# Performance work log

Hardware: AMD Instinct MI355X
Metric: run time of the kernel (lower is better)

## Reference

```python
import jax, jax.numpy as jnp
import numpy as np

IN, H, HC, HQ, OUT = 7, 64, 32, 16, 3  # input, shared hidden, cell hidden, head hidden, per-task out
B, S = 256, 2048


def setup_inputs() -> dict:
    key = jax.random.key(0)
    ks = iter(jax.random.split(key, 40))
    def p(shape, scale=0.1):
        return jax.random.normal(next(ks), shape, dtype=jnp.float32) * scale
    d = {}
    d['x'] = jax.random.normal(next(ks), (B, S, IN), dtype=jnp.float32)
    # shared LSTM (torch gate order i,f,g,o)
    d['W_ih_s'] = p((4 * H, IN)); d['W_hh_s'] = p((4 * H, H))
    d['b_ih_s'] = p((4 * H,));    d['b_hh_s'] = p((4 * H,))
    # attitude cell: input = [shared_h(64), x(7)]
    d['W_ih_a'] = p((4 * HC, H + IN)); d['W_hh_a'] = p((4 * HC, HC))
    d['b_ih_a'] = p((4 * HC,));        d['b_hh_a'] = p((4 * HC,))
    # velocity cell: input = [shared_h(64), delta_att(3), x(7)]
    d['W_ih_v'] = p((4 * HC, H + OUT + IN)); d['W_hh_v'] = p((4 * HC, HC))
    d['b_ih_v'] = p((4 * HC,));              d['b_hh_v'] = p((4 * HC,))
    # position cell: input = [shared_h(64), delta_vel(3)]
    d['W_ih_p'] = p((4 * HC, H + OUT)); d['W_hh_p'] = p((4 * HC, HC))
    d['b_ih_p'] = p((4 * HC,));         d['b_hh_p'] = p((4 * HC,))
    # per-task readout MLPs (dropout is identity in eval mode)
    d['Wa1'] = p((HQ, HC)); d['ba1'] = p((HQ,)); d['Wa2'] = p((OUT, HQ)); d['ba2'] = p((OUT,))
    d['Wv1'] = p((HQ, HC)); d['bv1'] = p((HQ,)); d['Wv2'] = p((OUT, HQ)); d['bv2'] = p((OUT,))
    d['Wp1'] = p((HQ, HC)); d['bp1'] = p((HQ,)); d['Wp2'] = p((OUT, HQ)); d['bp2'] = p((OUT,))
    return d


def lstm_cell(x, h, c, Wih, Whh, bih, bhh):
    z = x @ Wih.T + h @ Whh.T + bih + bhh
    i, f, g, o = jnp.split(z, 4, axis=-1)
    c = jax.nn.sigmoid(f) * c + jax.nn.sigmoid(i) * jnp.tanh(g)
    h = jax.nn.sigmoid(o) * jnp.tanh(c)
    return h, c


def mlp(h, W1, b1, W2, b2):
    return jax.nn.relu(h @ W1.T + b1) @ W2.T + b2


def reference(x, W_ih_s, W_hh_s, b_ih_s, b_hh_s,
              W_ih_a, W_hh_a, b_ih_a, b_hh_a,
              W_ih_v, W_hh_v, b_ih_v, b_hh_v,
              W_ih_p, W_hh_p, b_ih_p, b_hh_p,
              Wa1, ba1, Wa2, ba2, Wv1, bv1, Wv2, bv2, Wp1, bp1, Wp2, bp2):
    b = x.shape[0]
    z = lambda n: jnp.zeros((b, n), x.dtype)
    carry0 = (z(H), z(H), z(HC), z(HC), z(HC), z(HC), z(HC), z(HC))

    def step(carry, xt):
        hs, cs, ha, ca, hv, cv, hp, cp = carry
        hs, cs = lstm_cell(xt, hs, cs, W_ih_s, W_hh_s, b_ih_s, b_hh_s)
        ha, ca = lstm_cell(jnp.concatenate([hs, xt], -1), ha, ca,
                           W_ih_a, W_hh_a, b_ih_a, b_hh_a)
        d_att = mlp(ha, Wa1, ba1, Wa2, ba2)
        hv, cv = lstm_cell(jnp.concatenate([hs, jax.lax.stop_gradient(d_att), xt], -1),
                           hv, cv, W_ih_v, W_hh_v, b_ih_v, b_hh_v)
        d_vel = mlp(hv, Wv1, bv1, Wv2, bv2)
        hp, cp = lstm_cell(jnp.concatenate([hs, jax.lax.stop_gradient(d_vel)], -1),
                           hp, cp, W_ih_p, W_hh_p, b_ih_p, b_hh_p)
        d_pos = mlp(hp, Wp1, bp1, Wp2, bp2)
        out = jnp.concatenate([d_att, d_vel, d_pos], -1)  # [B, 9]
        return (hs, cs, ha, ca, hv, cv, hp, cp), out

    _, ys = jax.lax.scan(step, carry0, jnp.swapaxes(x, 0, 1))  # [S, B, 9]
    return jnp.swapaxes(ys, 0, 1)  # [B, S, 9]
```

## Files before the change

kernel.cpp:

```cpp
#include <hip/hip_runtime.h>

typedef unsigned int u32;

#define NIN 7
#define NB 256
#define NS 2048

__device__ __forceinline__ float fastrcp(float x){ return __builtin_amdgcn_rcpf(x); }
__device__ __forceinline__ float sigf(float x){ return fastrcp(1.f + __expf(-x)); }
__device__ __forceinline__ float tanhf_(float x){ return 1.f - 2.f*fastrcp(1.f + __expf(2.f*x)); }

__device__ __forceinline__ u32 pkh(float a, float b){
  unsigned short ua = __builtin_bit_cast(unsigned short, (_Float16)a);
  unsigned short ub = __builtin_bit_cast(unsigned short, (_Float16)b);
  return (u32)ua | ((u32)ub << 16);
}

template<int J>
__device__ __forceinline__ float rlf(float v){
  return __uint_as_float((unsigned)__builtin_amdgcn_readlane((int)__float_as_uint(v), J));
}
__device__ __forceinline__ float rlfv(float v, int j){
  return __uint_as_float((unsigned)__builtin_amdgcn_readlane((int)__float_as_uint(v), j));
}

__device__ __forceinline__ float mxl(float acc, u32 wp, float a){
  asm("v_fma_mix_f32 %0, %1, %2, %3 op_sel_hi:[1,0,0]"
      : "=v"(acc) : "v"(wp), "s"(a), "0"(acc));
  return acc;
}
__device__ __forceinline__ float mxh(float acc, u32 wp, float a){
  asm("v_fma_mix_f32 %0, %1, %2, %3 op_sel:[1,0,0] op_sel_hi:[1,0,0]"
      : "=v"(acc) : "v"(wp), "s"(a), "0"(acc));
  return acc;
}
__device__ __forceinline__ float mxlv(float acc, u32 wp, float a){
  asm("v_fma_mix_f32 %0, %1, %2, %3 op_sel_hi:[1,0,0]"
      : "=v"(acc) : "v"(wp), "v"(a), "0"(acc));
  return acc;
}
__device__ __forceinline__ float mxhv(float acc, u32 wp, float a){
  asm("v_fma_mix_f32 %0, %1, %2, %3 op_sel:[1,0,0] op_sel_hi:[1,0,0]"
      : "=v"(acc) : "v"(wp), "v"(a), "0"(acc));
  return acc;
}

__device__ __forceinline__ float gate4(float zi, float zf, float zg, float zo, float& c){
  c = sigf(zf)*c + sigf(zi)*tanhf_(zg);
  return sigf(zo)*tanhf_(c);
}

#define XD(a0, a1, KB, v0, v1) { \
  a0 = mxlv(a0, w[(KB)+0], (v0).x); a1 = mxhv(a1, w[(KB)+0], (v0).y); \
  a0 = mxlv(a0, w[(KB)+1], (v0).z); a1 = mxhv(a1, w[(KB)+1], (v0).w); \
  a0 = mxlv(a0, w[(KB)+2], (v1).x); a1 = mxhv(a1, w[(KB)+2], (v1).y); \
  a0 = mxlv(a0, w[(KB)+3], (v1).z); a1 = mxhv(a1, w[(KB)+3], (v1).w); }

#define LMX2(a0, a1, s0, s1, KA, KS, H4) { _Pragma("unroll") \
  for (int c_ = 0; c_ < 16; c_++){ \
    float4 h_ = (H4)[c_]; \
    a0 = mxlv(a0, w[(KA)+2*c_],   h_.x); a1 = mxhv(a1, w[(KA)+2*c_],   h_.y); \
    a0 = mxlv(a0, w[(KA)+2*c_+1], h_.z); a1 = mxhv(a1, w[(KA)+2*c_+1], h_.w); \
    s0 = mxlv(s0, w[(KS)+2*c_],   h_.x); s1 = mxhv(s1, w[(KS)+2*c_],   h_.y); \
    s0 = mxlv(s0, w[(KS)+2*c_+1], h_.z); s1 = mxhv(s1, w[(KS)+2*c_+1], h_.w); } }

#define LMX1(a0, a1, KA, H4) { _Pragma("unroll") \
  for (int c_ = 0; c_ < 16; c_++){ \
    float4 h_ = (H4)[c_]; \
    a0 = mxlv(a0, w[(KA)+2*c_],   h_.x); a1 = mxhv(a1, w[(KA)+2*c_],   h_.y); \
    a0 = mxlv(a0, w[(KA)+2*c_+1], h_.z); a1 = mxhv(a1, w[(KA)+2*c_+1], h_.w); } }

#define LMXH(z0, z1, KB, H4) { _Pragma("unroll") \
  for (int c_ = 0; c_ < 8; c_++){ \
    float4 h_ = (H4)[c_]; \
    z0 = mxlv(z0, w[(KB)+2*c_],   h_.x); z1 = mxhv(z1, w[(KB)+2*c_],   h_.y); \
    z0 = mxlv(z0, w[(KB)+2*c_+1], h_.z); z1 = mxhv(z1, w[(KB)+2*c_+1], h_.w); } }

#define MX2(a0, a1, s0, s1, KA, KS, SRC) { _Pragma("unroll") \
  for (int k_ = 0; k_ < 32; k_++){ \
    float e0_ = rlfv(SRC, 2*k_), e1_ = rlfv(SRC, 2*k_+1); \
    a0 = mxl(a0, w[(KA)+k_], e0_); a1 = mxh(a1, w[(KA)+k_], e1_); \
    s0 = mxl(s0, w[(KS)+k_], e0_); s1 = mxh(s1, w[(KS)+k_], e1_); } }

#define MX1(a0, a1, KA, SRC) { _Pragma("unroll") \
  for (int k_ = 0; k_ < 32; k_++){ \
    float e0_ = rlfv(SRC, 2*k_), e1_ = rlfv(SRC, 2*k_+1); \
    a0 = mxl(a0, w[(KA)+k_], e0_); a1 = mxh(a1, w[(KA)+k_], e1_); } }

#define MLPX(HS_, M1B, B1V, M2B, B2V, dres) { \
  float q0_ = (B1V), q1_ = 0.f, q2_ = 0.f, q3_ = 0.f; \
  _Pragma("unroll") \
  for (int j_ = 0; j_ < 16; j_++){ \
    float e0_ = rlfv(HS_, 2*j_), e1_ = rlfv(HS_, 2*j_+1); \
    if ((j_&1)==0){ q0_ = mxl(q0_, w[(M1B)+j_], e0_); q1_ = mxh(q1_, w[(M1B)+j_], e1_); } \
    else          { q2_ = mxl(q2_, w[(M1B)+j_], e0_); q3_ = mxh(q3_, w[(M1B)+j_], e1_); } } \
  float qq_ = fmaxf((q0_+q2_) + (q1_+q3_), 0.f); \
  float f0_ = (B2V), f1_ = 0.f, f2_ = 0.f, f3_ = 0.f; \
  _Pragma("unroll") \
  for (int j_ = 0; j_ < 8; j_++){ \
    float e0_ = rlfv(qq_, 2*j_), e1_ = rlfv(qq_, 2*j_+1); \
    if ((j_&1)==0){ f0_ = mxl(f0_, w[(M2B)+j_], e0_); f1_ = mxh(f1_, w[(M2B)+j_], e1_); } \
    else          { f2_ = mxl(f2_, w[(M2B)+j_], e0_); f3_ = mxh(f3_, w[(M2B)+j_], e1_); } } \
  dres = (f0_+f2_) + (f1_+f3_); }

__global__ __attribute__((amdgpu_flat_work_group_size(512,512), amdgpu_waves_per_eu(2,2)))
void mtinn_kernel(
    const float* __restrict__ x,
    const float* wihs, const float* whhs, const float* bihs, const float* bhhs,
    const float* wiha, const float* whha, const float* biha, const float* bhha,
    const float* wihv, const float* whhv, const float* bihv, const float* bhhv,
    const float* wihp, const float* whhp, const float* bihp, const float* bhhp,
    const float* wa1, const float* ba1, const float* wa2, const float* ba2,
    const float* wv1, const float* bv1, const float* wv2, const float* bv2,
    const float* wp1, const float* bp1, const float* wp2, const float* bp2,
    float* __restrict__ out)
{
  __shared__ __align__(16) float ZS[2][256];
  __shared__ __align__(16) float ZC[3][128];
  __shared__ __align__(16) float HS[64];
  __shared__ __align__(16) float HA[32], HV[32];
  __shared__ __align__(16) float HPb[2][32];
  __shared__ __align__(16) float XL[4][8];

  const int tid  = threadIdx.x;
  const int wave = tid >> 6, lane = tid & 63, l = lane & 31;
  const int b    = blockIdx.x;
  const float* xb = x + (size_t)b * NS * NIN;

  const bool isWin = (wave != 0 && wave != 4);
  const int  wc    = (wave==1||wave==7) ? 0 : (wave==2||wave==5) ? 1 : 2;
  const int  wrb   = (wave <= 3) ? 64 : 0;
  const bool isSh  = (wave==1 || wave==2 || wave==6 || wave==7);
  const int  qoff  = (wave==1) ? 0 : (wave==2) ? 64 : (wave==6) ? 128 : 192;
  const int  mi = lane & 15, mm = lane % 3;

  u32 w[88];
#pragma unroll
  for (int i = 0; i < 88; i++) w[i] = 0u;
  float b1a=0.f,b2a=0.f,b1v=0.f,b2v=0.f,b1p=0.f,b2p=0.f;

  if (isWin){
    const float* wih = (wc==0) ? wiha : (wc==1) ? wihv : wihp;
    const float* whh = (wc==0) ? whha : (wc==1) ? whhv : whhp;
    const float* bi  = (wc==0) ? biha : (wc==1) ? bihv : bihp;
    const float* bh  = (wc==0) ? bhha : (wc==1) ? bhhv : bhhp;
    const int L = (wc==0) ? 71 : (wc==1) ? 74 : 67;
    const int r = wrb + lane;
#pragma unroll
    for (int k=0;k<16;k++) w[k] = pkh(whh[r*32+2*k], whh[r*32+2*k+1]);
#pragma unroll
    for (int k=0;k<32;k++) w[16+k] = pkh(wih[r*L+2*k], wih[r*L+2*k+1]);
    const float bsum = bi[r] + bh[r];
    if (wc==0){
      w[48]=pkh(wih[r*L+64],wih[r*L+65]); w[49]=pkh(wih[r*L+66],wih[r*L+67]);
      w[50]=pkh(wih[r*L+68],wih[r*L+69]); w[51]=pkh(wih[r*L+70], bsum);
    } else if (wc==1){
      w[48]=pkh(wih[r*L+67],wih[r*L+68]); w[49]=pkh(wih[r*L+69],wih[r*L+70]);
      w[50]=pkh(wih[r*L+71],wih[r*L+72]); w[51]=pkh(wih[r*L+73], bsum);
    } else {
      w[51]=pkh(0.f, bsum);
    }
  }
  if (isSh){
    const int r = qoff + lane;
#pragma unroll
    for (int k=0;k<32;k++) w[52+k] = pkh(whhs[r*64+2*k], whhs[r*64+2*k+1]);
    w[84]=pkh(wihs[r*7+0],wihs[r*7+1]); w[85]=pkh(wihs[r*7+2],wihs[r*7+3]);
    w[86]=pkh(wihs[r*7+4],wihs[r*7+5]); w[87]=pkh(wihs[r*7+6], bihs[r]+bhhs[r]);
  }
  if (wave == 0){
#pragma unroll
    for (int k=0;k<16;k++){
      w[k]    = pkh(wa1[mi*32+2*k], wa1[mi*32+2*k+1]);
      w[16+k] = pkh(wv1[mi*32+2*k], wv1[mi*32+2*k+1]);
    }
#pragma unroll
    for (int k=0;k<8;k++){
      w[48+k] = pkh(wa2[mm*16+2*k], wa2[mm*16+2*k+1]);
      w[56+k] = pkh(wv2[mm*16+2*k], wv2[mm*16+2*k+1]);
    }
#pragma unroll
    for (int g=0; g<4; g++){
      int rr = g*32 + l;
      w[72+2*g]   = pkh(wihv[rr*74+64], wihv[rr*74+65]);
      w[72+2*g+1] = pkh(wihv[rr*74+66], 0.f);
      w[80+2*g]   = pkh(wihp[rr*67+64], wihp[rr*67+65]);
      w[80+2*g+1] = pkh(wihp[rr*67+66], 0.f);
    }
    b1a=ba1[mi]; b2a=ba2[mm]; b1v=bv1[mi]; b2v=bv2[mm];
  }
  if (wave == 4){
#pragma unroll
    for (int k=0;k<16;k++) w[k] = pkh(wp1[mi*32+2*k], wp1[mi*32+2*k+1]);
#pragma unroll
    for (int k=0;k<8;k++)  w[16+k] = pkh(wp2[mm*16+2*k], wp2[mm*16+2*k+1]);
    b1p=bp1[mi]; b2p=bp2[mm];
  }

  if (tid < 32) HA[tid]=0.f;
  else if (tid < 64)  HV[tid-32]=0.f;
  else if (tid < 96)  HPb[0][tid-64]=0.f;
  else if (tid < 128) HPb[1][tid-96]=0.f;
  if (tid < 8){
    XL[0][tid] = (tid<7) ? xb[tid]         : 1.f;
    XL[1][tid] = (tid<7) ? xb[NIN+tid]     : 1.f;
    XL[2][tid] = (tid<7) ? xb[2*NIN+tid]   : 1.f;
    XL[3][tid] = 1.f;
  }
  __syncthreads();

  if (isSh){
    const float4* X0 = (const float4*)XL[0];
    float4 xa = X0[0], xb4 = X0[1];
    float s0=0.f, s1=0.f; XD(s0,s1,84,xa,xb4);
    ZS[0][qoff + lane] = s0 + s1;
  }
  __syncthreads();

  float c_s = 0.f;
  float c_a = 0.f, c_v = 0.f, c_p = 0.f;
  float zpart = 0.f;

  if (isWin){
    float zi_=ZS[0][lane], zf_=ZS[0][64+lane], zg_=ZS[0][128+lane], zo_=ZS[0][192+lane];
    float hsv = gate4(zi_,zf_,zg_,zo_, c_s);
    const float4* X0 = (const float4*)XL[0];
    float4 xa = X0[0], xb4 = X0[1];
    float a0=0.f, a1=0.f; XD(a0,a1,48,xa,xb4);
    if (isSh){
      const float4* X1 = (const float4*)XL[1];
      float4 xc = X1[0], xd = X1[1];
      float s0=0.f, s1=0.f; XD(s0,s1,84,xc,xd);
      MX2(a0,a1,s0,s1,16,52,hsv);
      ZS[1][qoff + lane] = s0 + s1;
    } else {
      MX1(a0,a1,16,hsv);
    }
    zpart = a0 + a1;
  } else if (wave == 4){
    float zi_=ZS[0][lane], zf_=ZS[0][64+lane], zg_=ZS[0][128+lane], zo_=ZS[0][192+lane];
    gate4(zi_,zf_,zg_,zo_, c_s);
  }
  __syncthreads();

#pragma unroll 1
  for (int t = 0; t < NS; t++){
    float xpre = 0.f;
    if (wave == 0){
      if (lane < 7){
        const int tf = (t+3 < NS) ? t+3 : NS-1;
        xpre = xb[(size_t)tf*NIN + lane];
      }
    } else if (wave == 4){
      const float* Zsrc = ZS[(t+1)&1];
      float zi_=Zsrc[lane], zf_=Zsrc[64+lane], zg_=Zsrc[128+lane], zo_=Zsrc[192+lane];
      float hsv2 = gate4(zi_,zf_,zg_,zo_, c_s);
      HS[lane] = hsv2;
      if (t > 0){
        float hp_ = HPb[(t^1)&1][l];
        float dP; MLPX(hp_, 0, b1p, 16, b2p, dP);
        if (lane < 3) out[((size_t)b*NS + (t-1))*9 + 6 + lane] = dP;
      }
    } else {
      const float4* H4 = (const float4*)((wc==0) ? HA : (wc==1) ? HV : HPb[(t^1)&1]);
      float z0 = zpart, z1 = 0.f;
      LMXH(z0,z1,0,H4);
      ZC[wc][wrb + lane] = z0 + z1;
    }
    __syncthreads();

    if (wave == 0){
      __builtin_amdgcn_s_setprio(1);
      float zai=ZC[0][l], zaf=ZC[0][32+l], zag=ZC[0][64+l], zao=ZC[0][96+l];
      float zvi=ZC[1][l], zvf=ZC[1][32+l], zvg=ZC[1][64+l], zvo=ZC[1][96+l];
      float zpi=ZC[2][l], zpf=ZC[2][32+l], zpg=ZC[2][64+l], zpo=ZC[2][96+l];
      float* ob = out + ((size_t)b*NS + t)*9;
      float ha = gate4(zai,zaf,zag,zao, c_a);
      if (lane < 32) HA[lane] = ha;
      float dA; MLPX(ha, 0, b1a, 48, b2a, dA);
      if (lane < 3) ob[lane] = dA;
      float dx=rlf<0>(dA), dy=rlf<1>(dA), dz=rlf<2>(dA);
      zvi = mxl(zvi, w[72], dx); zvi = mxh(zvi, w[72], dy); zvi = mxl(zvi, w[73], dz);
      zvf = mxl(zvf, w[74], dx); zvf = mxh(zvf, w[74], dy); zvf = mxl(zvf, w[75], dz);
      zvg = mxl(zvg, w[76], dx); zvg = mxh(zvg, w[76], dy); zvg = mxl(zvg, w[77], dz);
      zvo = mxl(zvo, w[78], dx); zvo = mxh(zvo, w[78], dy); zvo = mxl(zvo, w[79], dz);
      float hv = gate4(zvi,zvf,zvg,zvo, c_v);
      if (lane < 32) HV[lane] = hv;
      float dV; MLPX(hv, 16, b1v, 56, b2v, dV);
      if (lane < 3) ob[3+lane] = dV;
      dx=rlf<0>(dV); dy=rlf<1>(dV); dz=rlf<2>(dV);
      zpi = mxl(zpi, w[80], dx); zpi = mxh(zpi, w[80], dy); zpi = mxl(zpi, w[81], dz);
      zpf = mxl(zpf, w[82], dx); zpf = mxh(zpf, w[82], dy); zpf = mxl(zpf, w[83], dz);
      zpg = mxl(zpg, w[84], dx); zpg = mxh(zpg, w[84], dy); zpg = mxl(zpg, w[85], dz);
      zpo = mxl(zpo, w[86], dx); zpo = mxh(zpo, w[86], dy); zpo = mxl(zpo, w[87], dz);
      float hp_ = gate4(zpi,zpf,zpg,zpo, c_p);
      if (lane < 32) HPb[t&1][lane] = hp_;
      __builtin_amdgcn_s_setprio(0);
      if (lane < 7) XL[(t+3)&3][lane] = xpre;
    } else if (isWin){
      const float4* H4 = (const float4*)HS;
      const float4* X1 = (const float4*)XL[(t+1)&3];
      float4 xa = X1[0], xb4 = X1[1];
      float a0=0.f, a1=0.f; XD(a0,a1,48,xa,xb4);
      if (isSh){
        const float4* X2 = (const float4*)XL[(t+2)&3];
        float4 xc = X2[0], xd = X2[1];
        float s0=0.f, s1=0.f; XD(s0,s1,84,xc,xd);
        LMX2(a0,a1,s0,s1,16,52,H4);
        ZS[t&1][qoff + lane] = s0 + s1;
      } else {
        LMX1(a0,a1,16,H4);
      }
      zpart = a0 + a1;
    }
    __syncthreads();
  }

  if (wave == 4){
    float hp_ = HPb[(NS-1)&1][l];
    float dP; MLPX(hp_, 0, b1p, 16, b2p, dP);
    if (lane < 3) out[((size_t)b*NS + (NS-1))*9 + 6 + lane] = dP;
  }
}

extern "C" void kernel_launch(void* const* d_in, const int* in_sizes, int n_in,
                              void* d_out, int out_size, void* d_ws, size_t ws_size,
                              hipStream_t stream) {
  (void)in_sizes; (void)n_in; (void)d_ws; (void)ws_size; (void)out_size;
  const float* X    = (const float*)d_in[0];
  const float* Wihs = (const float*)d_in[1];
  const float* Whhs = (const float*)d_in[2];
  const float* Bihs = (const float*)d_in[3];
  const float* Bhhs = (const float*)d_in[4];
  const float* Wiha = (const float*)d_in[5];
  const float* Whha = (const float*)d_in[6];
  const float* Biha = (const float*)d_in[7];
  const float* Bhha = (const float*)d_in[8];
  const float* Wihv = (const float*)d_in[9];
  const float* Whhv = (const float*)d_in[10];
  const float* Bihv = (const float*)d_in[11];
  const float* Bhhv = (const float*)d_in[12];
  const float* Wihp = (const float*)d_in[13];
  const float* Whhp = (const float*)d_in[14];
  const float* Bihp = (const float*)d_in[15];
  const float* Bhhp = (const float*)d_in[16];
  const float* Wa1  = (const float*)d_in[17];
  const float* Ba1  = (const float*)d_in[18];
  const float* Wa2  = (const float*)d_in[19];
  const float* Ba2  = (const float*)d_in[20];
  const float* Wv1  = (const float*)d_in[21];
  const float* Bv1  = (const float*)d_in[22];
  const float* Wv2  = (const float*)d_in[23];
  const float* Bv2  = (const float*)d_in[24];
  const float* Wp1  = (const float*)d_in[25];
  const float* Bp1  = (const float*)d_in[26];
  const float* Wp2  = (const float*)d_in[27];
  const float* Bp2  = (const float*)d_in[28];
  float* OUTP = (float*)d_out;

  mtinn_kernel<<<dim3(NB), dim3(512), 0, stream>>>(
      X, Wihs, Whhs, Bihs, Bhhs,
      Wiha, Whha, Biha, Bhha,
      Wihv, Whhv, Bihv, Bhhv,
      Wihp, Whhp, Bihp, Bhhp,
      Wa1, Ba1, Wa2, Ba2, Wv1, Bv1, Wv2, Bv2, Wp1, Bp1, Wp2, Bp2,
      OUTP);
}
```

Baseline: 2.935 ms.

## Rebalance shared-LSTM recurrent matvec across all cell waves with K-split partial sums

Instead of four cell waves each computing a full 64-row shared-LSTM gate block, the i/f/g rows are split across six cell waves by halves of the hidden dimension, with partial sums stored to separate LDS buffers and added by the gate wave. Wave 4 now also computes the output-gate rows of the shared LSTM. This evens out per-wave FMA work in the second phase to shorten the critical path and cuts the weight register array from 88 to 72 entries. The cost is extra LDS reads and adds in the gate step. The launch bounds attribute changes and the s_setprio priority boost for wave 0 is removed, which may hurt the serial head chain.

```diff
diff --git a/kernel.cpp b/kernel.cpp
--- a/kernel.cpp
+++ b/kernel.cpp
@@ -56,14 +56,6 @@
   a0 = mxlv(a0, w[(KB)+2], (v1).x); a1 = mxhv(a1, w[(KB)+2], (v1).y); \
   a0 = mxlv(a0, w[(KB)+3], (v1).z); a1 = mxhv(a1, w[(KB)+3], (v1).w); }
 
-#define LMX2(a0, a1, s0, s1, KA, KS, H4) { _Pragma("unroll") \
-  for (int c_ = 0; c_ < 16; c_++){ \
-    float4 h_ = (H4)[c_]; \
-    a0 = mxlv(a0, w[(KA)+2*c_],   h_.x); a1 = mxhv(a1, w[(KA)+2*c_],   h_.y); \
-    a0 = mxlv(a0, w[(KA)+2*c_+1], h_.z); a1 = mxhv(a1, w[(KA)+2*c_+1], h_.w); \
-    s0 = mxlv(s0, w[(KS)+2*c_],   h_.x); s1 = mxhv(s1, w[(KS)+2*c_],   h_.y); \
-    s0 = mxlv(s0, w[(KS)+2*c_+1], h_.z); s1 = mxhv(s1, w[(KS)+2*c_+1], h_.w); } }
-
 #define LMX1(a0, a1, KA, H4) { _Pragma("unroll") \
   for (int c_ = 0; c_ < 16; c_++){ \
     float4 h_ = (H4)[c_]; \
@@ -76,16 +68,20 @@
     z0 = mxlv(z0, w[(KB)+2*c_],   h_.x); z1 = mxhv(z1, w[(KB)+2*c_],   h_.y); \
     z0 = mxlv(z0, w[(KB)+2*c_+1], h_.z); z1 = mxhv(z1, w[(KB)+2*c_+1], h_.w); } }
 
-#define MX2(a0, a1, s0, s1, KA, KS, SRC) { _Pragma("unroll") \
-  for (int k_ = 0; k_ < 32; k_++){ \
-    float e0_ = rlfv(SRC, 2*k_), e1_ = rlfv(SRC, 2*k_+1); \
-    a0 = mxl(a0, w[(KA)+k_], e0_); a1 = mxh(a1, w[(KA)+k_], e1_); \
-    s0 = mxl(s0, w[(KS)+k_], e0_); s1 = mxh(s1, w[(KS)+k_], e1_); } }
-
 #define MX1(a0, a1, KA, SRC) { _Pragma("unroll") \
   for (int k_ = 0; k_ < 32; k_++){ \
     float e0_ = rlfv(SRC, 2*k_), e1_ = rlfv(SRC, 2*k_+1); \
     a0 = mxl(a0, w[(KA)+k_], e0_); a1 = mxh(a1, w[(KA)+k_], e1_); } }
+
+#define MXH16(z0, z1, KB, SRC) { _Pragma("unroll") \
+  for (int k_ = 0; k_ < 16; k_++){ \
+    float e0_ = rlfv(SRC, 2*k_), e1_ = rlfv(SRC, 2*k_+1); \
+    z0 = mxl(z0, w[(KB)+k_], e0_); z1 = mxh(z1, w[(KB)+k_], e1_); } }
+
+#define MXH16HI(z0, z1, KB, SRC) { _Pragma("unroll") \
+  for (int k_ = 0; k_ < 16; k_++){ \
+    float e0_ = rlfv(SRC, 32+2*k_), e1_ = rlfv(SRC, 33+2*k_); \
+    z0 = mxl(z0, w[(KB)+k_], e0_); z1 = mxh(z1, w[(KB)+k_], e1_); } }
 
 #define MLPX(HS_, M1B, B1V, M2B, B2V, dres) { \
   float q0_ = (B1V), q1_ = 0.f, q2_ = 0.f, q3_ = 0.f; \
@@ -103,8 +99,7 @@
     else          { f2_ = mxl(f2_, w[(M2B)+j_], e0_); f3_ = mxh(f3_, w[(M2B)+j_], e1_); } } \
   dres = (f0_+f2_) + (f1_+f3_); }
 
-__global__ __attribute__((amdgpu_flat_work_group_size(512,512), amdgpu_waves_per_eu(2,2)))
-void mtinn_kernel(
+__global__ __launch_bounds__(512, 1) void mtinn_kernel(
     const float* __restrict__ x,
     const float* wihs, const float* whhs, const float* bihs, const float* bhhs,
     const float* wiha, const float* whha, const float* biha, const float* bhha,
@@ -115,7 +110,9 @@
     const float* wp1, const float* bp1, const float* wp2, const float* bp2,
     float* __restrict__ out)
 {
-  __shared__ __align__(16) float ZS[2][256];
+  __shared__ __align__(16) float ZSL[2][192];
+  __shared__ __align__(16) float ZSH[2][192];
+  __shared__ __align__(16) float ZSO[2][64];
   __shared__ __align__(16) float ZC[3][128];
   __shared__ __align__(16) float HS[64];
   __shared__ __align__(16) float HA[32], HV[32];
@@ -130,13 +127,13 @@
   const bool isWin = (wave != 0 && wave != 4);
   const int  wc    = (wave==1||wave==7) ? 0 : (wave==2||wave==5) ? 1 : 2;
   const int  wrb   = (wave <= 3) ? 64 : 0;
-  const bool isSh  = (wave==1 || wave==2 || wave==6 || wave==7);
-  const int  qoff  = (wave==1) ? 0 : (wave==2) ? 64 : (wave==6) ? 128 : 192;
+  const bool shHi  = (wave >= 5);
+  const int  qoff  = (wave==1||wave==5) ? 0 : (wave==2||wave==6) ? 64 : 128;
   const int  mi = lane & 15, mm = lane % 3;
 
-  u32 w[88];
-#pragma unroll
-  for (int i = 0; i < 88; i++) w[i] = 0u;
+  u32 w[72];
+#pragma unroll
+  for (int i = 0; i < 72; i++) w[i] = 0u;
   float b1a=0.f,b2a=0.f,b1v=0.f,b2v=0.f,b1p=0.f,b2p=0.f;
 
   if (isWin){
@@ -160,13 +157,16 @@
     } else {
       w[51]=pkh(0.f, bsum);
     }
-  }
-  if (isSh){
-    const int r = qoff + lane;
-#pragma unroll
-    for (int k=0;k<32;k++) w[52+k] = pkh(whhs[r*64+2*k], whhs[r*64+2*k+1]);
-    w[84]=pkh(wihs[r*7+0],wihs[r*7+1]); w[85]=pkh(wihs[r*7+2],wihs[r*7+3]);
-    w[86]=pkh(wihs[r*7+4],wihs[r*7+5]); w[87]=pkh(wihs[r*7+6], bihs[r]+bhhs[r]);
+    const int rs = qoff + lane;
+    if (!shHi){
+#pragma unroll
+      for (int k=0;k<16;k++) w[52+k] = pkh(whhs[rs*64+2*k], whhs[rs*64+2*k+1]);
+    } else {
+#pragma unroll
+      for (int k=0;k<16;k++) w[52+k] = pkh(whhs[rs*64+32+2*k], whhs[rs*64+33+2*k]);
+      w[68]=pkh(wihs[rs*7+0],wihs[rs*7+1]); w[69]=pkh(wihs[rs*7+2],wihs[rs*7+3]);
+      w[70]=pkh(wihs[rs*7+4],wihs[rs*7+5]); w[71]=pkh(wihs[rs*7+6], bihs[rs]+bhhs[rs]);
+    }
   }
   if (wave == 0){
 #pragma unroll
@@ -176,16 +176,16 @@
     }
 #pragma unroll
     for (int k=0;k<8;k++){
-      w[48+k] = pkh(wa2[mm*16+2*k], wa2[mm*16+2*k+1]);
-      w[56+k] = pkh(wv2[mm*16+2*k], wv2[mm*16+2*k+1]);
+      w[32+k] = pkh(wa2[mm*16+2*k], wa2[mm*16+2*k+1]);
+      w[40+k] = pkh(wv2[mm*16+2*k], wv2[mm*16+2*k+1]);
     }
 #pragma unroll
     for (int g=0; g<4; g++){
       int rr = g*32 + l;
-      w[72+2*g]   = pkh(wihv[rr*74+64], wihv[rr*74+65]);
-      w[72+2*g+1] = pkh(wihv[rr*74+66], 0.f);
-      w[80+2*g]   = pkh(wihp[rr*67+64], wihp[rr*67+65]);
-      w[80+2*g+1] = pkh(wihp[rr*67+66], 0.f);
+      w[48+2*g]   = pkh(wihv[rr*74+64], wihv[rr*74+65]);
+      w[48+2*g+1] = pkh(wihv[rr*74+66], 0.f);
+      w[56+2*g]   = pkh(wihp[rr*67+64], wihp[rr*67+65]);
+      w[56+2*g+1] = pkh(wihp[rr*67+66], 0.f);
     }
     b1a=ba1[mi]; b2a=ba2[mm]; b1v=bv1[mi]; b2v=bv2[mm];
   }
@@ -194,6 +194,11 @@
     for (int k=0;k<16;k++) w[k] = pkh(wp1[mi*32+2*k], wp1[mi*32+2*k+1]);
 #pragma unroll
     for (int k=0;k<8;k++)  w[16+k] = pkh(wp2[mm*16+2*k], wp2[mm*16+2*k+1]);
+    const int ro = 192 + lane;
+#pragma unroll
+    for (int k=0;k<32;k++) w[24+k] = pkh(whhs[ro*64+2*k], whhs[ro*64+2*k+1]);
+    w[56]=pkh(wihs[ro*7+0],wihs[ro*7+1]); w[57]=pkh(wihs[ro*7+2],wihs[ro*7+3]);
+    w[58]=pkh(wihs[ro*7+4],wihs[ro*7+5]); w[59]=pkh(wihs[ro*7+6], bihs[ro]+bhhs[ro]);
     b1p=bp1[mi]; b2p=bp2[mm];
   }
 
@@ -209,11 +214,19 @@
   }
   __syncthreads();
 
-  if (isSh){
+  {
     const float4* X0 = (const float4*)XL[0];
     float4 xa = X0[0], xb4 = X0[1];
-    float s0=0.f, s1=0.f; XD(s0,s1,84,xa,xb4);
-    ZS[0][qoff + lane] = s0 + s1;
+    if (isWin && !shHi) ZSL[0][qoff + lane] = 0.f;
+    if (isWin && shHi){
+      float s0=0.f, s1=0.f; XD(s0,s1,68,xa,xb4);
+      ZSH[0][qoff + lane] = s0 + s1;
+      ZSL[1][qoff + lane] = 0.f;
+    }
+    if (wave == 4){
+      float o0=0.f, o1=0.f; XD(o0,o1,56,xa,xb4);
+      ZSO[0][lane] = o0 + o1;
+    }
   }
   __syncthreads();
 
@@ -221,25 +234,38 @@
   float c_a = 0.f, c_v = 0.f, c_p = 0.f;
   float zpart = 0.f;
 
-  if (isWin){
-    float zi_=ZS[0][lane], zf_=ZS[0][64+lane], zg_=ZS[0][128+lane], zo_=ZS[0][192+lane];
-    float hsv = gate4(zi_,zf_,zg_,zo_, c_s);
+  {
     const float4* X0 = (const float4*)XL[0];
-    float4 xa = X0[0], xb4 = X0[1];
-    float a0=0.f, a1=0.f; XD(a0,a1,48,xa,xb4);
-    if (isSh){
-      const float4* X1 = (const float4*)XL[1];
+    const float4* X1 = (const float4*)XL[1];
+    if (isWin){
+      float zi_=ZSL[0][lane]+ZSH[0][lane], zf_=ZSL[0][64+lane]+ZSH[0][64+lane];
+      float zg_=ZSL[0][128+lane]+ZSH[0][128+lane], zo_=ZSO[0][lane];
+      float cd = 0.f;
+      float hsv = gate4(zi_,zf_,zg_,zo_, cd);
+      float4 xa = X0[0], xb4 = X0[1];
+      float a0=0.f, a1=0.f; XD(a0,a1,48,xa,xb4);
+      MX1(a0,a1,16,hsv);
+      zpart = a0 + a1;
+      float s0=0.f, s1=0.f;
+      if (!shHi){
+        MXH16(s0,s1,52,hsv);
+        ZSL[1][qoff + lane] = s0 + s1;
+      } else {
+        MXH16HI(s0,s1,52,hsv);
+        float4 xc = X1[0], xd = X1[1];
+        XD(s0,s1,68,xc,xd);
+        ZSH[1][qoff + lane] = s0 + s1;
+      }
+    } else if (wave == 4){
+      float zi_=ZSL[0][lane]+ZSH[0][lane], zf_=ZSL[0][64+lane]+ZSH[0][64+lane];
+      float zg_=ZSL[0][128+lane]+ZSH[0][128+lane], zo_=ZSO[0][lane];
+      float hsv = gate4(zi_,zf_,zg_,zo_, c_s);
+      float o0=0.f, o1=0.f;
+      MX1(o0,o1,24,hsv);
       float4 xc = X1[0], xd = X1[1];
-      float s0=0.f, s1=0.f; XD(s0,s1,84,xc,xd);
-      MX2(a0,a1,s0,s1,16,52,hsv);
-      ZS[1][qoff + lane] = s0 + s1;
-    } else {
-      MX1(a0,a1,16,hsv);
-    }
-    zpart = a0 + a1;
-  } else if (wave == 4){
-    float zi_=ZS[0][lane], zf_=ZS[0][64+lane], zg_=ZS[0][128+lane], zo_=ZS[0][192+lane];
-    gate4(zi_,zf_,zg_,zo_, c_s);
+      XD(o0,o1,56,xc,xd);
+      ZSO[1][lane] = o0 + o1;
+    }
   }
   __syncthreads();
 
@@ -252,8 +278,9 @@
         xpre = xb[(size_t)tf*NIN + lane];
       }
     } else if (wave == 4){
-      const float* Zsrc = ZS[(t+1)&1];
-      float zi_=Zsrc[lane], zf_=Zsrc[64+lane], zg_=Zsrc[128+lane], zo_=Zsrc[192+lane];
+      const int rb = (t+1)&1;
+      float zi_=ZSL[rb][lane]+ZSH[rb][lane], zf_=ZSL[rb][64+lane]+ZSH[rb][64+lane];
+      float zg_=ZSL[rb][128+lane]+ZSH[rb][128+lane], zo_=ZSO[rb][lane];
       float hsv2 = gate4(zi_,zf_,zg_,zo_, c_s);
       HS[lane] = hsv2;
       if (t > 0){
@@ -270,48 +297,57 @@
     __syncthreads();
 
     if (wave == 0){
-      __builtin_amdgcn_s_setprio(1);
       float zai=ZC[0][l], zaf=ZC[0][32+l], zag=ZC[0][64+l], zao=ZC[0][96+l];
       float zvi=ZC[1][l], zvf=ZC[1][32+l], zvg=ZC[1][64+l], zvo=ZC[1][96+l];
       float zpi=ZC[2][l], zpf=ZC[2][32+l], zpg=ZC[2][64+l], zpo=ZC[2][96+l];
       float* ob = out + ((size_t)b*NS + t)*9;
       float ha = gate4(zai,zaf,zag,zao, c_a);
       if (lane < 32) HA[lane] = ha;
-      float dA; MLPX(ha, 0, b1a, 48, b2a, dA);
+      float dA; MLPX(ha, 0, b1a, 32, b2a, dA);
       if (lane < 3) ob[lane] = dA;
       float dx=rlf<0>(dA), dy=rlf<1>(dA), dz=rlf<2>(dA);
-      zvi = mxl(zvi, w[72], dx); zvi = mxh(zvi, w[72], dy); zvi = mxl(zvi, w[73], dz);
-      zvf = mxl(zvf, w[74], dx); zvf = mxh(zvf, w[74], dy); zvf = mxl(zvf, w[75], dz);
-      zvg = mxl(zvg, w[76], dx); zvg = mxh(zvg, w[76], dy); zvg = mxl(zvg, w[77], dz);
-      zvo = mxl(zvo, w[78], dx); zvo = mxh(zvo, w[78], dy); zvo = mxl(zvo, w[79], dz);
+      zvi = mxl(zvi, w[48], dx); zvi = mxh(zvi, w[48], dy); zvi = mxl(zvi, w[49], dz);
+      zvf = mxl(zvf, w[50], dx); zvf = mxh(zvf, w[50], dy); zvf = mxl(zvf, w[51], dz);
+      zvg = mxl(zvg, w[52], dx); zvg = mxh(zvg, w[52], dy); zvg = mxl(zvg, w[53], dz);
+      zvo = mxl(zvo, w[54], dx); zvo = mxh(zvo, w[54], dy); zvo = mxl(zvo, w[55], dz);
       float hv = gate4(zvi,zvf,zvg,zvo, c_v);
       if (lane < 32) HV[lane] = hv;
-      float dV; MLPX(hv, 16, b1v, 56, b2v, dV);
+      float dV; MLPX(hv, 16, b1v, 40, b2v, dV);
       if (lane < 3) ob[3+lane] = dV;
       dx=rlf<0>(dV); dy=rlf<1>(dV); dz=rlf<2>(dV);
-      zpi = mxl(zpi, w[80], dx); zpi = mxh(zpi, w[80], dy); zpi = mxl(zpi, w[81], dz);
-      zpf = mxl(zpf, w[82], dx); zpf = mxh(zpf, w[82], dy); zpf = mxl(zpf, w[83], dz);
-      zpg = mxl(zpg, w[84], dx); zpg = mxh(zpg, w[84], dy); zpg = mxl(zpg, w[85], dz);
-      zpo = mxl(zpo, w[86], dx); zpo = mxh(zpo, w[86], dy); zpo = mxl(zpo, w[87], dz);
+      zpi = mxl(zpi, w[56], dx); zpi = mxh(zpi, w[56], dy); zpi = mxl(zpi, w[57], dz);
+      zpf = mxl(zpf, w[58], dx); zpf = mxh(zpf, w[58], dy); zpf = mxl(zpf, w[59], dz);
+      zpg = mxl(zpg, w[60], dx); zpg = mxh(zpg, w[60], dy); zpg = mxl(zpg, w[61], dz);
+      zpo = mxl(zpo, w[62], dx); zpo = mxh(zpo, w[62], dy); zpo = mxl(zpo, w[63], dz);
       float hp_ = gate4(zpi,zpf,zpg,zpo, c_p);
       if (lane < 32) HPb[t&1][lane] = hp_;
-      __builtin_amdgcn_s_setprio(0);
       if (lane < 7) XL[(t+3)&3][lane] = xpre;
-    } else if (isWin){
+    } else if (wave == 4){
+      const float4* H4 = (const float4*)HS;
+      float o0=0.f, o1=0.f;
+      LMX1(o0,o1,24,H4);
+      const float4* X2 = (const float4*)XL[(t+2)&3];
+      float4 xc = X2[0], xd = X2[1];
+      XD(o0,o1,56,xc,xd);
+      ZSO[t&1][lane] = o0 + o1;
+    } else {
       const float4* H4 = (const float4*)HS;
       const float4* X1 = (const float4*)XL[(t+1)&3];
       float4 xa = X1[0], xb4 = X1[1];
       float a0=0.f, a1=0.f; XD(a0,a1,48,xa,xb4);
-      if (isSh){
+      LMX1(a0,a1,16,H4);
+      zpart = a0 + a1;
+      float s0=0.f, s1=0.f;
+      if (!shHi){
+        LMXH(s0,s1,52,H4);
+        ZSL[t&1][qoff + lane] = s0 + s1;
+      } else {
+        LMXH(s0,s1,52,H4+8);
         const float4* X2 = (const float4*)XL[(t+2)&3];
         float4 xc = X2[0], xd = X2[1];
-        float s0=0.f, s1=0.f; XD(s0,s1,84,xc,xd);
-        LMX2(a0,a1,s0,s1,16,52,H4);
-        ZS[t&1][qoff + lane] = s0 + s1;
-      } else {
-        LMX1(a0,a1,16,H4);
+        XD(s0,s1,68,xc,xd);
+        ZSH[t&1][qoff + lane] = s0 + s1;
       }
-      zpart = a0 + a1;
     }
     __syncthreads();
   }
```

Result: no change. 2.948 ms (+0.4%).
